# Performance work log

Measured on AMD Instinct MI355X. Metric: run time of the kernel, lower is better.

Reference implementation:

```python
import math
import jax, jax.numpy as jnp
import numpy as np

B, S, D_MODEL, H = 2, 2048, 1024, 16
HEAD_DIM = D_MODEL // H
NUM_BUCKETS = 32
MAX_DISTANCE = 128
SCALING = HEAD_DIM ** (-0.5)


def setup_inputs() -> dict:
    key = jax.random.key(0)
    ks = jax.random.split(key, 6)
    inp = {
        "hidden_states": jax.random.normal(ks[0], (B, S, D_MODEL), jnp.float32),
        "Wq": jax.random.normal(ks[1], (D_MODEL, D_MODEL), jnp.float32) * (D_MODEL ** -0.5),
        "Wk": jax.random.normal(ks[2], (D_MODEL, D_MODEL), jnp.float32) * (D_MODEL ** -0.5),
        "Wv": jax.random.normal(ks[3], (D_MODEL, D_MODEL), jnp.float32) * (D_MODEL ** -0.5),
        "Wo": jax.random.normal(ks[4], (D_MODEL, D_MODEL), jnp.float32) * (D_MODEL ** -0.5),
        "rel_emb": jax.random.normal(ks[5], (NUM_BUCKETS, H), jnp.float32),
    }
    return inp


def _relative_position_bucket(relative_position, num_buckets=NUM_BUCKETS, max_distance=MAX_DISTANCE):
    # bidirectional (encoder) bucketing, matches T5 _relative_position_bucket
    num_buckets = num_buckets // 2
    relative_buckets = (relative_position > 0).astype(jnp.int32) * num_buckets
    relative_position = jnp.abs(relative_position)
    max_exact = num_buckets // 2
    is_small = relative_position < max_exact
    rp_f = jnp.maximum(relative_position, 1).astype(jnp.float32)  # guard log(0)
    rel_if_large = max_exact + (
        jnp.log(rp_f / max_exact) / math.log(max_distance / max_exact) * (num_buckets - max_exact)
    ).astype(jnp.int32)
    rel_if_large = jnp.minimum(rel_if_large, num_buckets - 1)
    relative_buckets = relative_buckets + jnp.where(is_small, relative_position, rel_if_large)
    return relative_buckets


def compute_bias(rel_emb, q_len, k_len):
    context_position = jnp.arange(q_len)[:, None]
    memory_position = jnp.arange(k_len)[None, :]
    relative_position = memory_position - context_position  # [q, k]
    buckets = _relative_position_bucket(relative_position)
    values = rel_emb[buckets]                  # [q, k, H]
    return jnp.transpose(values, (2, 0, 1))[None]  # [1, H, q, k]


def reference(hidden_states, Wq, Wk, Wv, Wo, rel_emb):
    b, s, _ = hidden_states.shape

    def shape(x):  # [b, s, d_model] -> [b, H, s, head_dim]
        return x.reshape(b, s, H, HEAD_DIM).transpose(0, 2, 1, 3)

    q = shape(hidden_states @ Wq.T)
    k = shape(hidden_states @ Wk.T)
    v = shape(hidden_states @ Wv.T)

    position_bias = compute_bias(rel_emb, s, s)            # [1, H, s, s]
    scores = jnp.einsum("bhqd,bhkd->bhqk", q, k) * SCALING + position_bias
    attn = jax.nn.softmax(scores, axis=-1)
    ctx = jnp.einsum("bhqk,bhkd->bhqd", attn, v)           # [b, H, s, head_dim]
    ctx = ctx.transpose(0, 2, 1, 3).reshape(b, s, D_MODEL)
    return ctx @ Wo.T
```

## Files before the change

### kernel.cpp

```cpp
#include <hip/hip_runtime.h>
#include <math.h>

#define H_    16
#define S_    2048
#define DH_   64
#define DM_   1024
#define NTOK_ 4096
#define NBIAS_ 4095

typedef __attribute__((ext_vector_type(8))) short short8;
typedef __attribute__((ext_vector_type(4))) float f32x4;

#define MFMA16(a, b, c) __builtin_amdgcn_mfma_f32_16x16x32_bf16((a), (b), (c), 0, 0, 0)

__device__ __forceinline__ ushort f2bf(float f) {
  union { float f; unsigned u; } x; x.f = f;
  unsigned r = (x.u + 0x7FFFu + ((x.u >> 16) & 1u)) >> 16;
  return (ushort)r;
}
__device__ __forceinline__ ushort f2bf_fast(float f) {
  union { float f; unsigned u; } x; x.f = f;
  return (ushort)((x.u + 0x8000u) >> 16);
}

__device__ __forceinline__ void ldg16_lds(const ushort* g, ushort* l) {
  __builtin_amdgcn_global_load_lds(
      (const __attribute__((address_space(1))) unsigned int*)g,
      (__attribute__((address_space(3))) unsigned int*)l, 16, 0, 0);
}

__global__ void cast_bf16_k(const float* __restrict__ in, ushort* __restrict__ out, int n) {
  int i = (blockIdx.x * blockDim.x + threadIdx.x) * 4;
  if (i >= n) return;
  const float4 v = *(const float4*)(in + i);
  ushort4 o;
  o.x = f2bf(v.x); o.y = f2bf(v.y); o.z = f2bf(v.z); o.w = f2bf(v.w);
  *(ushort4*)(out + i) = o;
}

__global__ void build_bias_k(const float* __restrict__ rel_emb, float* __restrict__ biasTab) {
  int d = blockIdx.x * blockDim.x + threadIdx.x;
  if (d >= NBIAS_) return;
  int rp = d - (S_ - 1);
  int ret = (rp > 0) ? 16 : 0;
  int arp = rp < 0 ? -rp : rp;
  int bucket;
  if (arp < 8) {
    bucket = ret + arp;
  } else {
    float t = logf((float)arp * 0.125f);
    t = t / 2.772588722239781f;
    t = t * 8.0f;
    int large = 8 + (int)t;
    if (large > 15) large = 15;
    bucket = ret + large;
  }
  for (int h = 0; h < H_; ++h)
    biasTab[h * NBIAS_ + d] = rel_emb[bucket * H_ + h];
}

__device__ __forceinline__ void gemm_core(
    const ushort* __restrict__ gA, const ushort* __restrict__ gB,
    ushort* As, ushort* Bs, f32x4 (&acc)[4][4],
    int m0, int n0, int wave, int lane)
{
  const int l15 = lane & 15, quad = lane >> 4;
  const int wm = wave >> 1, wn = wave & 1;
  const int srow = lane >> 3;
  const int sw = ((lane & 7) ^ (lane >> 3)) * 8;
  const int px = l15 & 7;

  for (int k0 = 0; k0 < DM_; k0 += 64) {
    __syncthreads();
#pragma unroll
    for (int i = 0; i < 8; ++i) {
      int c = wave * 8 + i;
      if (c < 16)
        ldg16_lds(gA + (size_t)(m0 + c * 8 + srow) * DM_ + k0 + sw, As + c * 512);
      else
        ldg16_lds(gB + (size_t)(n0 + (c - 16) * 8 + srow) * DM_ + k0 + sw, Bs + (c - 16) * 512);
    }
    __syncthreads();
#pragma unroll
    for (int kk = 0; kk < 2; ++kk) {
      short8 af[4], bfr[4];
#pragma unroll
      for (int mi = 0; mi < 4; ++mi)
        af[mi] = *(const short8*)&As[(wm * 64 + mi * 16 + l15) * 64 + (((kk * 4 + quad) ^ px)) * 8];
#pragma unroll
      for (int ni = 0; ni < 4; ++ni)
        bfr[ni] = *(const short8*)&Bs[(wn * 64 + ni * 16 + l15) * 64 + (((kk * 4 + quad) ^ px)) * 8];
#pragma unroll
      for (int mi = 0; mi < 4; ++mi)
#pragma unroll
        for (int ni = 0; ni < 4; ++ni)
          acc[mi][ni] = MFMA16(af[mi], bfr[ni], acc[mi][ni]);
    }
  }
}

__global__ __launch_bounds__(256) void gemm_qkv_k(
    const ushort* __restrict__ X,
    const ushort* __restrict__ Wq, const ushort* __restrict__ Wk, const ushort* __restrict__ Wv,
    ushort* __restrict__ Q, ushort* __restrict__ K, ushort* __restrict__ Vt)
{
  __shared__ __align__(16) ushort sh[17408];
  ushort* As = sh;
  ushort* Bs = sh + 8192;
  const int z = blockIdx.z;
  const ushort* __restrict__ W = (z == 0) ? Wq : (z == 1) ? Wk : Wv;
  const int tid = threadIdx.x;
  const int wave = tid >> 6, lane = tid & 63;
  const int l15 = lane & 15, quad = lane >> 4;
  const int wm = wave >> 1, wn = wave & 1;
  const int m0 = blockIdx.y * 128;
  const int n0 = blockIdx.x * 128;

  f32x4 acc[4][4];
#pragma unroll
  for (int mi = 0; mi < 4; ++mi)
#pragma unroll
    for (int ni = 0; ni < 4; ++ni) acc[mi][ni] = (f32x4){0.f, 0.f, 0.f, 0.f};

  gemm_core(X, W, As, Bs, acc, m0, n0, wave, lane);

  if (z < 2) {
    ushort* dst = (z == 0) ? Q : K;
#pragma unroll
    for (int mi = 0; mi < 4; ++mi)
#pragma unroll
      for (int ni = 0; ni < 4; ++ni)
#pragma unroll
        for (int r = 0; r < 4; ++r) {
          int m = m0 + wm * 64 + mi * 16 + quad * 4 + r;
          int n = n0 + wn * 64 + ni * 16 + l15;
          int b = m >> 11, s = m & (S_ - 1);
          int hh = n >> 6, dd = n & 63;
          dst[((size_t)(b * H_ + hh) * S_ + s) * DH_ + dd] = f2bf(acc[mi][ni][r]);
        }
  } else {
    __syncthreads();
#pragma unroll
    for (int mi = 0; mi < 4; ++mi)
#pragma unroll
      for (int ni = 0; ni < 4; ++ni) {
        int n = wn * 64 + ni * 16 + l15;
        int m = wm * 64 + mi * 16 + quad * 4;
        ushort4 w4;
        w4.x = f2bf(acc[mi][ni][0]); w4.y = f2bf(acc[mi][ni][1]);
        w4.z = f2bf(acc[mi][ni][2]); w4.w = f2bf(acc[mi][ni][3]);
        *(ushort4*)&sh[n * 136 + m] = w4;
      }
    __syncthreads();
    const int b = m0 >> 11, s0 = m0 & (S_ - 1);
#pragma unroll
    for (int p = 0; p < 8; ++p) {
      int task = p * 256 + tid;
      int n = task >> 4, mc = (task & 15) * 8;
      int col = n0 + n, hh = col >> 6, dd = col & 63;
      *(short8*)(Vt + ((size_t)(b * H_ + hh) * DH_ + dd) * S_ + s0 + mc) =
          *(const short8*)&sh[n * 136 + mc];
    }
  }
}

__global__ __launch_bounds__(256) void gemm_out_k(
    const ushort* __restrict__ A, const ushort* __restrict__ W, float* __restrict__ out)
{
  __shared__ __align__(16) ushort sh[16384];
  ushort* As = sh;
  ushort* Bs = sh + 8192;
  const int tid = threadIdx.x;
  const int wave = tid >> 6, lane = tid & 63;
  const int l15 = lane & 15, quad = lane >> 4;
  const int wm = wave >> 1, wn = wave & 1;
  const int m0 = blockIdx.y * 128;
  const int n0 = blockIdx.x * 128;

  f32x4 acc[4][4];
#pragma unroll
  for (int mi = 0; mi < 4; ++mi)
#pragma unroll
    for (int ni = 0; ni < 4; ++ni) acc[mi][ni] = (f32x4){0.f, 0.f, 0.f, 0.f};

  gemm_core(A, W, As, Bs, acc, m0, n0, wave, lane);

#pragma unroll
  for (int mi = 0; mi < 4; ++mi)
#pragma unroll
    for (int ni = 0; ni < 4; ++ni)
#pragma unroll
      for (int r = 0; r < 4; ++r) {
        int m = m0 + wm * 64 + mi * 16 + quad * 4 + r;
        int n = n0 + wn * 64 + ni * 16 + l15;
        out[(size_t)m * DM_ + n] = acc[mi][ni][r];
      }
}

__global__ __launch_bounds__(256, 2) void attn_k(
    const ushort* __restrict__ Q, const ushort* __restrict__ K, const ushort* __restrict__ Vt,
    const float* __restrict__ biasTab, ushort* __restrict__ Ctx)
{
  __shared__ __align__(16) ushort KV[8192];
  __shared__ float bias_s[2111];
  ushort* Ks = KV;
  ushort* Vs = KV + 4096;

  const int tid = threadIdx.x;
  const int wave = tid >> 6, lane = tid & 63;
  const int l15 = lane & 15, quad = lane >> 4;
  const int bh = blockIdx.y;
  const int h = bh & (H_ - 1);
  const int b = bh >> 4;
  const int qb = blockIdx.x * 64;
  const int srow = lane >> 3;
  const int sw = ((lane & 7) ^ (lane >> 3)) * 8;

  const f32x4 zero4 = {0.f, 0.f, 0.f, 0.f};

  for (int i = tid; i < 2111; i += 256)
    bias_s[i] = biasTab[h * NBIAS_ + 1984 - qb + i];

  const ushort* Qh = Q  + (size_t)bh * S_ * DH_;
  const ushort* Kh = K  + (size_t)bh * S_ * DH_;
  const ushort* Vh = Vt + (size_t)bh * DH_ * S_;

  short8 qf[4][2];
#pragma unroll
  for (int nf = 0; nf < 4; ++nf)
#pragma unroll
    for (int kk = 0; kk < 2; ++kk)
      qf[nf][kk] = *(const short8*)(Qh + (size_t)(qb + nf * 16 + l15) * DH_ + kk * 32 + quad * 8);

  short8 oneh;
#pragma unroll
  for (int i = 0; i < 8; ++i) oneh[i] = (i < 4) ? (short)0x3F80 : (short)0;

  f32x4 of[4][4];
#pragma unroll
  for (int nf = 0; nf < 4; ++nf)
#pragma unroll
    for (int nt = 0; nt < 4; ++nt) of[nf][nt] = zero4;
  f32x4 ls[4];
#pragma unroll
  for (int nf = 0; nf < 4; ++nf) ls[nf] = zero4;

  const int kidx = (wave * 16 + l15) * 64;
  const int vslot = wave * 2 + (quad >> 1);

  for (int kt = 0; kt < S_; kt += 64) {
    __syncthreads();
#pragma unroll
    for (int i = 0; i < 2; ++i) {
      int c = wave * 2 + i;
      ldg16_lds(Kh + (size_t)(kt + c * 8 + srow) * DH_ + sw, Ks + c * 512);
      ldg16_lds(Vh + (size_t)(c * 8 + srow) * S_ + kt + sw, Vs + c * 512);
    }
    __syncthreads();

    short8 kf0 = *(const short8*)&Ks[kidx + ((quad ^ (l15 & 7))) * 8];
    short8 kf1 = *(const short8*)&Ks[kidx + (((4 + quad) ^ (l15 & 7))) * 8];
    f32x4 sc[4];
#pragma unroll
    for (int nf = 0; nf < 4; ++nf) {
      sc[nf] = MFMA16(kf0, qf[nf][0], zero4);
      sc[nf] = MFMA16(kf1, qf[nf][1], sc[nf]);
    }

    short8 pf[4];
    const int ib = kt + wave * 16 + quad * 4 + 63 - l15;
#pragma unroll
    for (int nf = 0; nf < 4; ++nf) {
      const int i0 = ib - nf * 16;
      pf[nf][0] = (short)f2bf_fast(__expf(sc[nf][0] * 0.125f + bias_s[i0]));
      pf[nf][1] = (short)f2bf_fast(__expf(sc[nf][1] * 0.125f + bias_s[i0 + 1]));
      pf[nf][2] = (short)f2bf_fast(__expf(sc[nf][2] * 0.125f + bias_s[i0 + 2]));
      pf[nf][3] = (short)f2bf_fast(__expf(sc[nf][3] * 0.125f + bias_s[i0 + 3]));
      pf[nf][4] = 0; pf[nf][5] = 0; pf[nf][6] = 0; pf[nf][7] = 0;
    }

#pragma unroll
    for (int nf = 0; nf < 4; ++nf) ls[nf] = MFMA16(pf[nf], oneh, ls[nf]);
#pragma unroll
    for (int nt = 0; nt < 4; ++nt) {
      ushort4 v4 = *(const ushort4*)&Vs[(nt * 16 + l15) * 64 +
                                        ((vslot ^ (l15 & 7))) * 8 + (quad & 1) * 4];
      short8 vf;
      vf[0] = (short)v4.x; vf[1] = (short)v4.y; vf[2] = (short)v4.z; vf[3] = (short)v4.w;
      vf[4] = 0; vf[5] = 0; vf[6] = 0; vf[7] = 0;
#pragma unroll
      for (int nf = 0; nf < 4; ++nf)
        of[nf][nt] = MFMA16(pf[nf], vf, of[nf][nt]);
    }
  }

  __syncthreads();
  float* red = (float*)KV;
#pragma unroll
  for (int mi = 0; mi < 4; ++mi) {
    if (wave) {
      int base = ((wave - 1) * 64 + lane) * 21;
#pragma unroll
      for (int nt = 0; nt < 4; ++nt)
#pragma unroll
        for (int r = 0; r < 4; ++r) red[base + nt * 4 + r] = of[mi][nt][r];
#pragma unroll
      for (int r = 0; r < 4; ++r) red[base + 16 + r] = ls[mi][r];
    }
    __syncthreads();
    if (wave == 0) {
#pragma unroll
      for (int w = 1; w < 4; ++w) {
        int base = ((w - 1) * 64 + lane) * 21;
#pragma unroll
        for (int nt = 0; nt < 4; ++nt)
#pragma unroll
          for (int r = 0; r < 4; ++r) of[mi][nt][r] += red[base + nt * 4 + r];
#pragma unroll
        for (int r = 0; r < 4; ++r) ls[mi][r] += red[base + 16 + r];
      }
#pragma unroll
      for (int nt = 0; nt < 4; ++nt)
#pragma unroll
        for (int r = 0; r < 4; ++r) {
          int t = b * S_ + qb + mi * 16 + quad * 4 + r;
          Ctx[(size_t)t * DM_ + h * 64 + nt * 16 + l15] = f2bf(of[mi][nt][r] / ls[mi][r]);
        }
    }
    __syncthreads();
  }
}

extern "C" void kernel_launch(void* const* d_in, const int* in_sizes, int n_in,
                              void* d_out, int out_size, void* d_ws, size_t ws_size,
                              hipStream_t stream) {
  const float* hs  = (const float*)d_in[0];
  const float* Wq  = (const float*)d_in[1];
  const float* Wk  = (const float*)d_in[2];
  const float* Wv  = (const float*)d_in[3];
  const float* Wo  = (const float*)d_in[4];
  const float* rel = (const float*)d_in[5];
  float* out = (float*)d_out;

  ushort* Xb  = (ushort*)d_ws;
  ushort* Wqb = Xb  + (size_t)NTOK_ * DM_;
  ushort* Wkb = Wqb + (size_t)DM_ * DM_;
  ushort* Wvb = Wkb + (size_t)DM_ * DM_;
  ushort* Wob = Wvb + (size_t)DM_ * DM_;
  ushort* Qd  = Wob + (size_t)DM_ * DM_;
  ushort* Kd  = Qd  + (size_t)NTOK_ * DM_;
  ushort* Vtd = Kd  + (size_t)NTOK_ * DM_;
  float* biasTab = (float*)(Vtd + (size_t)NTOK_ * DM_);
  ushort* Ctx = Xb;

  cast_bf16_k<<<4096, 256, 0, stream>>>(hs, Xb, NTOK_ * DM_);
  cast_bf16_k<<<1024, 256, 0, stream>>>(Wq, Wqb, DM_ * DM_);
  cast_bf16_k<<<1024, 256, 0, stream>>>(Wk, Wkb, DM_ * DM_);
  cast_bf16_k<<<1024, 256, 0, stream>>>(Wv, Wvb, DM_ * DM_);
  cast_bf16_k<<<1024, 256, 0, stream>>>(Wo, Wob, DM_ * DM_);
  build_bias_k<<<16, 256, 0, stream>>>(rel, biasTab);

  gemm_qkv_k<<<dim3(8, 32, 3), 256, 0, stream>>>(Xb, Wqb, Wkb, Wvb, Qd, Kd, Vtd);
  attn_k<<<dim3(S_ / 64, 2 * H_), 256, 0, stream>>>(Qd, Kd, Vtd, biasTab, Ctx);
  gemm_out_k<<<dim3(8, 32), 256, 0, stream>>>(Ctx, Wob, out);
}
```

Baseline: 242.4 us.

## Fuse prep kernels, read bias from global, use exp2 with prescaled bias

Merges the five cast launches and the bias-table build into one prep kernel, removing five launches. The bias table is prescaled by log2(e) so the attention kernel can use exp2f with a single fma. The attention kernel drops its LDS bias staging and reads bias straight from global (L1/L2) through a per-lane pointer. P is packed to bf16 with a byte permute and V fragments are assembled with 32-bit moves. Global bias loads in the inner loop may add latency compared with LDS reads.

```diff
diff --git a/kernel.cpp b/kernel.cpp
--- a/kernel.cpp
+++ b/kernel.cpp
@@ -12,15 +12,18 @@
 typedef __attribute__((ext_vector_type(4))) float f32x4;
 
 #define MFMA16(a, b, c) __builtin_amdgcn_mfma_f32_16x16x32_bf16((a), (b), (c), 0, 0, 0)
+#define LOG2E_DIV8 0.18033688011112042f
 
 __device__ __forceinline__ ushort f2bf(float f) {
   union { float f; unsigned u; } x; x.f = f;
   unsigned r = (x.u + 0x7FFFu + ((x.u >> 16) & 1u)) >> 16;
   return (ushort)r;
 }
-__device__ __forceinline__ ushort f2bf_fast(float f) {
-  union { float f; unsigned u; } x; x.f = f;
-  return (ushort)((x.u + 0x8000u) >> 16);
+
+__device__ __forceinline__ unsigned bpack(float hi, float lo) {
+  union { float f; unsigned u; } a, b;
+  a.f = hi; b.f = lo;
+  return __builtin_amdgcn_perm(a.u + 0x8000u, b.u + 0x8000u, 0x07060302u);
 }
 
 __device__ __forceinline__ void ldg16_lds(const ushort* g, ushort* l) {
@@ -29,34 +32,46 @@
       (__attribute__((address_space(3))) unsigned int*)l, 16, 0, 0);
 }
 
-__global__ void cast_bf16_k(const float* __restrict__ in, ushort* __restrict__ out, int n) {
-  int i = (blockIdx.x * blockDim.x + threadIdx.x) * 4;
-  if (i >= n) return;
-  const float4 v = *(const float4*)(in + i);
-  ushort4 o;
-  o.x = f2bf(v.x); o.y = f2bf(v.y); o.z = f2bf(v.z); o.w = f2bf(v.w);
-  *(ushort4*)(out + i) = o;
-}
-
-__global__ void build_bias_k(const float* __restrict__ rel_emb, float* __restrict__ biasTab) {
-  int d = blockIdx.x * blockDim.x + threadIdx.x;
-  if (d >= NBIAS_) return;
-  int rp = d - (S_ - 1);
-  int ret = (rp > 0) ? 16 : 0;
-  int arp = rp < 0 ? -rp : rp;
-  int bucket;
-  if (arp < 8) {
-    bucket = ret + arp;
+__global__ void prep_k(const float* __restrict__ hs,
+                       const float* __restrict__ Wq, const float* __restrict__ Wk,
+                       const float* __restrict__ Wv, const float* __restrict__ Wo,
+                       const float* __restrict__ rel,
+                       ushort* __restrict__ Xb, ushort* __restrict__ Wqb,
+                       ushort* __restrict__ Wkb, ushort* __restrict__ Wvb,
+                       ushort* __restrict__ Wob, float* __restrict__ biasTab) {
+  const int bid = blockIdx.x;
+  if (bid < 8192) {
+    int i = (bid * 256 + threadIdx.x) * 4;
+    const float* src; ushort* dst; int off;
+    if (i < 4194304)      { src = hs; dst = Xb;  off = i; }
+    else if (i < 5242880) { src = Wq; dst = Wqb; off = i - 4194304; }
+    else if (i < 6291456) { src = Wk; dst = Wkb; off = i - 5242880; }
+    else if (i < 7340032) { src = Wv; dst = Wvb; off = i - 6291456; }
+    else                  { src = Wo; dst = Wob; off = i - 7340032; }
+    const float4 v = *(const float4*)(src + off);
+    ushort4 o;
+    o.x = f2bf(v.x); o.y = f2bf(v.y); o.z = f2bf(v.z); o.w = f2bf(v.w);
+    *(ushort4*)(dst + off) = o;
   } else {
-    float t = logf((float)arp * 0.125f);
-    t = t / 2.772588722239781f;
-    t = t * 8.0f;
-    int large = 8 + (int)t;
-    if (large > 15) large = 15;
-    bucket = ret + large;
-  }
-  for (int h = 0; h < H_; ++h)
-    biasTab[h * NBIAS_ + d] = rel_emb[bucket * H_ + h];
+    int d = (bid - 8192) * 256 + threadIdx.x;
+    if (d >= NBIAS_) return;
+    int rp = d - (S_ - 1);
+    int ret = (rp > 0) ? 16 : 0;
+    int arp = rp < 0 ? -rp : rp;
+    int bucket;
+    if (arp < 8) {
+      bucket = ret + arp;
+    } else {
+      float t = logf((float)arp * 0.125f);
+      t = t / 2.772588722239781f;
+      t = t * 8.0f;
+      int large = 8 + (int)t;
+      if (large > 15) large = 15;
+      bucket = ret + large;
+    }
+    for (int h = 0; h < H_; ++h)
+      biasTab[h * NBIAS_ + d] = rel[bucket * H_ + h] * 1.4426950408889634f;
+  }
 }
 
 __device__ __forceinline__ void gemm_core(
@@ -202,7 +217,6 @@
     const float* __restrict__ biasTab, ushort* __restrict__ Ctx)
 {
   __shared__ __align__(16) ushort KV[8192];
-  __shared__ float bias_s[2111];
   ushort* Ks = KV;
   ushort* Vs = KV + 4096;
 
@@ -218,12 +232,11 @@
 
   const f32x4 zero4 = {0.f, 0.f, 0.f, 0.f};
 
-  for (int i = tid; i < 2111; i += 256)
-    bias_s[i] = biasTab[h * NBIAS_ + 1984 - qb + i];
-
   const ushort* Qh = Q  + (size_t)bh * S_ * DH_;
   const ushort* Kh = K  + (size_t)bh * S_ * DH_;
   const ushort* Vh = Vt + (size_t)bh * DH_ * S_;
+
+  const float* bp = biasTab + h * NBIAS_ + 2047 - qb + wave * 16 + quad * 4 - l15;
 
   short8 qf[4][2];
 #pragma unroll
@@ -268,26 +281,29 @@
     }
 
     short8 pf[4];
-    const int ib = kt + wave * 16 + quad * 4 + 63 - l15;
 #pragma unroll
     for (int nf = 0; nf < 4; ++nf) {
-      const int i0 = ib - nf * 16;
-      pf[nf][0] = (short)f2bf_fast(__expf(sc[nf][0] * 0.125f + bias_s[i0]));
-      pf[nf][1] = (short)f2bf_fast(__expf(sc[nf][1] * 0.125f + bias_s[i0 + 1]));
-      pf[nf][2] = (short)f2bf_fast(__expf(sc[nf][2] * 0.125f + bias_s[i0 + 2]));
-      pf[nf][3] = (short)f2bf_fast(__expf(sc[nf][3] * 0.125f + bias_s[i0 + 3]));
-      pf[nf][4] = 0; pf[nf][5] = 0; pf[nf][6] = 0; pf[nf][7] = 0;
+      const float* bnf = bp + kt - nf * 16;
+      float p0 = exp2f(fmaf(sc[nf][0], LOG2E_DIV8, bnf[0]));
+      float p1 = exp2f(fmaf(sc[nf][1], LOG2E_DIV8, bnf[1]));
+      float p2 = exp2f(fmaf(sc[nf][2], LOG2E_DIV8, bnf[2]));
+      float p3 = exp2f(fmaf(sc[nf][3], LOG2E_DIV8, bnf[3]));
+      union { short8 v; unsigned u[4]; } P;
+      P.u[0] = bpack(p1, p0);
+      P.u[1] = bpack(p3, p2);
+      P.u[2] = 0; P.u[3] = 0;
+      pf[nf] = P.v;
     }
 
 #pragma unroll
     for (int nf = 0; nf < 4; ++nf) ls[nf] = MFMA16(pf[nf], oneh, ls[nf]);
 #pragma unroll
     for (int nt = 0; nt < 4; ++nt) {
-      ushort4 v4 = *(const ushort4*)&Vs[(nt * 16 + l15) * 64 +
-                                        ((vslot ^ (l15 & 7))) * 8 + (quad & 1) * 4];
-      short8 vf;
-      vf[0] = (short)v4.x; vf[1] = (short)v4.y; vf[2] = (short)v4.z; vf[3] = (short)v4.w;
-      vf[4] = 0; vf[5] = 0; vf[6] = 0; vf[7] = 0;
+      const uint2 v2 = *(const uint2*)&Vs[(nt * 16 + l15) * 64 +
+                                          ((vslot ^ (l15 & 7))) * 8 + (quad & 1) * 4];
+      union { short8 v; unsigned u[4]; } V;
+      V.u[0] = v2.x; V.u[1] = v2.y; V.u[2] = 0; V.u[3] = 0;
+      short8 vf = V.v;
 #pragma unroll
       for (int nf = 0; nf < 4; ++nf)
         of[nf][nt] = MFMA16(pf[nf], vf, of[nf][nt]);
@@ -353,13 +369,8 @@
   float* biasTab = (float*)(Vtd + (size_t)NTOK_ * DM_);
   ushort* Ctx = Xb;
 
-  cast_bf16_k<<<4096, 256, 0, stream>>>(hs, Xb, NTOK_ * DM_);
-  cast_bf16_k<<<1024, 256, 0, stream>>>(Wq, Wqb, DM_ * DM_);
-  cast_bf16_k<<<1024, 256, 0, stream>>>(Wk, Wkb, DM_ * DM_);
-  cast_bf16_k<<<1024, 256, 0, stream>>>(Wv, Wvb, DM_ * DM_);
-  cast_bf16_k<<<1024, 256, 0, stream>>>(Wo, Wob, DM_ * DM_);
-  build_bias_k<<<16, 256, 0, stream>>>(rel, biasTab);
-
+  prep_k<<<8208, 256, 0, stream>>>(hs, Wq, Wk, Wv, Wo, rel,
+                                   Xb, Wqb, Wkb, Wvb, Wob, biasTab);
   gemm_qkv_k<<<dim3(8, 32, 3), 256, 0, stream>>>(Xb, Wqb, Wkb, Wvb, Qd, Kd, Vtd);
   attn_k<<<dim3(S_ / 64, 2 * H_), 256, 0, stream>>>(Qd, Kd, Vtd, biasTab, Ctx);
   gemm_out_k<<<dim3(8, 32), 256, 0, stream>>>(Ctx, Wob, out);
```

Result: slower. 255.9 us (+5.5%).
